# Performance work log

Hardware: AMD Instinct MI355X
Metric: run time of the kernel (lower is better)

## Reference

```python
import jax, jax.numpy as jnp
import numpy as np

B, N, C = 4, 2048, 512
H, D, L = 8, 64, 64  # num_heads, per-head dim, lunchbox_dim
SCALE = max(D, L) ** (-0.5)

def setup_inputs() -> dict:
    key = jax.random.key(0)
    k1, k2, k3, k4 = jax.random.split(key, 4)
    x = jax.random.normal(k1, (B, N, C), dtype=jnp.float32)
    v = jax.random.normal(k2, (N, H, L), dtype=jnp.float32) * (1.0 / np.sqrt(N))
    qkv = jax.random.normal(k3, (C, D * 2 * H), dtype=jnp.float32) * (1.0 / np.sqrt(C))
    proj = jax.random.normal(k4, (H * L, D), dtype=jnp.float32) * (1.0 / np.sqrt(H * L))
    return {"x": x, "v": v, "qkv": qkv, "proj": proj}

def reference(x, v, qkv, proj):
    # x: [B,N,C] -> [B,N,H,2,D]
    h = jnp.einsum('bnc,cd->bnd', x, qkv).reshape(B, N, H, 2, D)
    q = h[:, :, :, 0, :]  # [B,N,H,D]
    k = h[:, :, :, 1, :]  # [B,N,H,D]
    # attention scores [B,H,N,N]; NOTE: original code calls tf.nn.softmax but
    # discards the result, so no softmax is applied (faithful reproduction).
    attn = jnp.einsum('bnhd,bmhd->bhnm', q, k) * SCALE
    # contract with batch-independent lunchbox V: [B,H,N,N] x [N,H,L] -> [B,N,H,L]
    res = jnp.einsum('bhnm,mhl->bnhl', attn, v).reshape(B, N, H * L)
    out = jnp.einsum('bnc,cd->bnd', res, proj)  # [B,N,D]
    return out
```

## Files before the change

kernel.cpp:

```cpp
#include <hip/hip_runtime.h>
#include <hip/hip_bf16.h>


using f32x4 = __attribute__((ext_vector_type(4))) float;
using s16x8 = __attribute__((ext_vector_type(8))) short;

__device__ __forceinline__ unsigned short f2bf(float f) {
  unsigned int i;
  __builtin_memcpy(&i, &f, 4);
  unsigned int lsb = (i >> 16) & 1u;
  i += 0x7fffu + lsb;
  return (unsigned short)(i >> 16);
}
__device__ __forceinline__ float bf2f(unsigned short u) {
  unsigned int i = ((unsigned int)u) << 16;
  float f;
  __builtin_memcpy(&f, &i, 4);
  return f;
}
__device__ __forceinline__ void async_cp16(const void* g, void* l) {
  __builtin_amdgcn_global_load_lds((const __attribute__((address_space(1))) void*)g,
                                   (__attribute__((address_space(3))) void*)l, 16, 0, 0);
}

__global__ void k_prep(const float* __restrict__ x, const float* __restrict__ qkv,
                       unsigned short* __restrict__ xb, unsigned short* __restrict__ qkvT) {
  const int id = blockIdx.x;
  const int tid = threadIdx.x;
  if (id < 2048) {
    size_t i = ((size_t)id * 256 + tid) * 8;
    f32x4 a = *(const f32x4*)(x + i);
    f32x4 b = *(const f32x4*)(x + i + 4);
    ushort4 lo, hi;
    lo.x = f2bf(a[0]); lo.y = f2bf(a[1]); lo.z = f2bf(a[2]); lo.w = f2bf(a[3]);
    hi.x = f2bf(b[0]); hi.y = f2bf(b[1]); hi.z = f2bf(b[2]); hi.w = f2bf(b[3]);
    *(ushort4*)(xb + i) = lo;
    *(ushort4*)(xb + i + 4) = hi;
  } else {
    __shared__ float tile[32][33];
    const int idx = id - 2048;
    const int j0 = (idx & 31) * 32;
    const int c0 = (idx >> 5) * 32;
    const int tx = tid & 31, ty = tid >> 5;
#pragma unroll
    for (int i = 0; i < 32; i += 8)
      tile[ty + i][tx] = qkv[(size_t)(c0 + ty + i) * 1024 + j0 + tx];
    __syncthreads();
    const int h = j0 >> 7, s = (j0 >> 6) & 1, d0 = j0 & 63;
    const int jp0 = s * 512 + h * 64 + d0;
#pragma unroll
    for (int i = 0; i < 32; i += 8)
      qkvT[(size_t)(jp0 + ty + i) * 512 + c0 + tx] = f2bf(tile[tx][ty + i]);
  }
}

__global__ __launch_bounds__(512) void k_gemm1(
    const unsigned short* __restrict__ A,
    const unsigned short* __restrict__ Bt,
    unsigned short* __restrict__ Qws,
    unsigned short* __restrict__ Kws) {
  __shared__ unsigned short As[128 * 64];
  __shared__ unsigned short Bs[128 * 64];
  const int m0 = blockIdx.x * 128;
  const int n0 = blockIdx.y * 128;
  const int tid = threadIdx.x;
  const int lane = tid & 63;
  const int wave = tid >> 6;
  const int wm = wave >> 1, wn = wave & 1;

  f32x4 acc[2][4] = {};

  const int rlane = lane >> 3;
  const int clane = (lane & 7) * 8;

  for (int kt = 0; kt < 512; kt += 64) {
    __syncthreads();
#pragma unroll
    for (int i = 0; i < 2; ++i) {
      async_cp16(A + (size_t)(m0 + i * 64 + wave * 8 + rlane) * 512 + kt + clane,
                 As + (i * 64 + wave * 8) * 64);
      async_cp16(Bt + (size_t)(n0 + i * 64 + wave * 8 + rlane) * 512 + kt + clane,
                 Bs + (i * 64 + wave * 8) * 64);
    }
    __syncthreads();
#pragma unroll
    for (int kk = 0; kk < 64; kk += 32) {
      s16x8 af[2], bfr[4];
#pragma unroll
      for (int i = 0; i < 2; ++i)
        af[i] = *(const s16x8*)(As + (wm * 32 + i * 16 + (lane & 15)) * 64 + kk + (lane >> 4) * 8);
#pragma unroll
      for (int j = 0; j < 4; ++j)
        bfr[j] = *(const s16x8*)(Bs + (wn * 64 + j * 16 + (lane & 15)) * 64 + kk + (lane >> 4) * 8);
#pragma unroll
      for (int i = 0; i < 2; ++i)
#pragma unroll
        for (int j = 0; j < 4; ++j)
          acc[i][j] = __builtin_amdgcn_mfma_f32_16x16x32_bf16(af[i], bfr[j], acc[i][j], 0, 0, 0);
    }
  }
  const int n_base = n0 + wn * 64;
#pragma unroll
  for (int i = 0; i < 2; ++i) {
    int grow = m0 + wm * 32 + i * 16 + (lane >> 4) * 4;
#pragma unroll
    for (int j = 0; j < 4; ++j) {
      int gcol = n_base + j * 16 + (lane & 15);
      unsigned short* dst;
      float scale;
      if (gcol < 512) { dst = Qws; scale = 0.125f; }
      else            { dst = Kws; gcol -= 512; scale = 1.0f; }
#pragma unroll
      for (int r = 0; r < 4; ++r)
        dst[(size_t)(grow + r) * 512 + gcol] = f2bf(acc[i][j][r] * scale);
    }
  }
}

__global__ void k_kv_partial(const unsigned short* __restrict__ Kws,
                             const float* __restrict__ v,
                             float* __restrict__ KVp) {
  const int wg = blockIdx.x;
  const int chunk = wg & 15;
  const int h = (wg >> 4) & 7;
  const int b = wg >> 7;
  __shared__ unsigned short Ks[128 * 64];
  __shared__ float Vs[128 * 64];
  const int tid = threadIdx.x;
  const int lane = tid & 63;
  const int wave = tid >> 6;
  const int n0 = chunk * 128;
  {
    const int r = wave * 32 + (lane >> 3);
    const int c = (lane & 7) * 8;
#pragma unroll
    for (int i = 0; i < 4; ++i)
      async_cp16(Kws + (size_t)(b * 2048 + n0 + r + i * 8) * 512 + h * 64 + c,
                 Ks + (wave * 32 + i * 8) * 64);
  }
  {
    const int r = wave * 32 + (lane >> 4);
    const int c = (lane & 15) * 4;
#pragma unroll
    for (int i = 0; i < 8; ++i)
      async_cp16(v + (size_t)(n0 + r + i * 4) * 512 + h * 64 + c,
                 Vs + (wave * 32 + i * 4) * 64);
  }
  __syncthreads();
  const int dq0 = (tid & 15) * 4;
  const int l0 = (tid >> 4) * 4;
  float acc[4][4] = {};
#pragma unroll 4
  for (int n = 0; n < 128; ++n) {
    ushort4 ku = *(const ushort4*)(Ks + n * 64 + dq0);
    f32x4 va = *(const f32x4*)(Vs + n * 64 + l0);
    float ka[4] = {bf2f(ku.x), bf2f(ku.y), bf2f(ku.z), bf2f(ku.w)};
#pragma unroll
    for (int a = 0; a < 4; ++a)
#pragma unroll
      for (int c = 0; c < 4; ++c)
        acc[a][c] += ka[a] * va[c];
  }
  float* dst = KVp + (size_t)wg * 4096;
#pragma unroll
  for (int a = 0; a < 4; ++a) {
    f32x4 o;
    o[0] = acc[a][0]; o[1] = acc[a][1]; o[2] = acc[a][2]; o[3] = acc[a][3];
    *(f32x4*)(dst + (dq0 + a) * 64 + l0) = o;
  }
}

__global__ void k_kv_reduce_w(const float* __restrict__ KVp,
                              const float* __restrict__ proj,
                              unsigned short* __restrict__ WcatT) {
  const int bh = blockIdx.x;
  const int h = bh & 7;
  const int b = bh >> 3;
  __shared__ float kv[64 * 65];
  __shared__ float pj[64 * 64];
  const int tid = threadIdx.x;
#pragma unroll
  for (int j = 0; j < 16; ++j) {
    int e = tid + j * 256;
    float s = 0.f;
#pragma unroll
    for (int c = 0; c < 16; ++c)
      s += KVp[((size_t)bh * 16 + c) * 4096 + e];
    kv[(e >> 6) * 65 + (e & 63)] = s;
  }
#pragma unroll
  for (int j = 0; j < 16; ++j) {
    int e = tid + j * 256;
    pj[e] = proj[(size_t)(h * 64 + (e >> 6)) * 64 + (e & 63)];
  }
  __syncthreads();
  const int dq = tid >> 2;
  const int d0 = (tid & 3) * 16;
  f32x4 w[4] = {};
  for (int l = 0; l < 64; ++l) {
    float kvv = kv[dq * 65 + l];
#pragma unroll
    for (int jj = 0; jj < 4; ++jj) {
      f32x4 p4 = *(const f32x4*)(pj + l * 64 + d0 + jj * 4);
      w[jj] += kvv * p4;
    }
  }
#pragma unroll
  for (int jj = 0; jj < 4; ++jj)
#pragma unroll
    for (int q = 0; q < 4; ++q)
      WcatT[(size_t)(b * 64 + d0 + jj * 4 + q) * 512 + h * 64 + dq] = f2bf(w[jj][q]);
}

__global__ __launch_bounds__(64) void k_gemm2(
    const unsigned short* __restrict__ Qws,
    const unsigned short* __restrict__ WcatT,
    float* __restrict__ out) {
  const int m0 = blockIdx.x * 16;
  const int lane = threadIdx.x;
  const unsigned short* Bb = WcatT + (size_t)(m0 >> 11) * 64 * 512;
  const int arow = lane & 15;
  const int koff = (lane >> 4) * 8;
  f32x4 acc[4] = {};
#pragma unroll
  for (int kk = 0; kk < 16; ++kk) {
    s16x8 af = *(const s16x8*)(Qws + (size_t)(m0 + arow) * 512 + kk * 32 + koff);
#pragma unroll
    for (int j = 0; j < 4; ++j) {
      s16x8 bf = *(const s16x8*)(Bb + (size_t)(j * 16 + arow) * 512 + kk * 32 + koff);
      acc[j] = __builtin_amdgcn_mfma_f32_16x16x32_bf16(af, bf, acc[j], 0, 0, 0);
    }
  }
  const int grow = m0 + (lane >> 4) * 4;
#pragma unroll
  for (int j = 0; j < 4; ++j) {
    int gcol = j * 16 + arow;
#pragma unroll
    for (int r = 0; r < 4; ++r)
      out[(size_t)(grow + r) * 64 + gcol] = acc[j][r];
  }
}

extern "C" void kernel_launch(void* const* d_in, const int* in_sizes, int n_in,
                              void* d_out, int out_size, void* d_ws, size_t ws_size,
                              hipStream_t stream) {
  const float* x    = (const float*)d_in[0];
  const float* v    = (const float*)d_in[1];
  const float* qkv  = (const float*)d_in[2];
  const float* proj = (const float*)d_in[3];
  float* out = (float*)d_out;

  char* ws = (char*)d_ws;
  unsigned short* xb   = (unsigned short*)ws; ws += (size_t)8192 * 512 * 2;
  unsigned short* qkvT = (unsigned short*)ws; ws += (size_t)1024 * 512 * 2;
  unsigned short* Qws  = (unsigned short*)ws; ws += (size_t)8192 * 512 * 2;
  unsigned short* Kws  = (unsigned short*)ws; ws += (size_t)8192 * 512 * 2;
  float*          KVp  = (float*)ws;          ws += (size_t)512 * 4096 * 4;
  unsigned short* Wc   = (unsigned short*)ws; ws += (size_t)4 * 64 * 512 * 2;

  hipLaunchKernelGGL(k_prep, dim3(2560), dim3(256), 0, stream, x, qkv, xb, qkvT);
  hipLaunchKernelGGL(k_gemm1, dim3(64, 8), dim3(512), 0, stream, xb, qkvT, Qws, Kws);
  hipLaunchKernelGGL(k_kv_partial, dim3(512), dim3(256), 0, stream, Kws, v, KVp);
  hipLaunchKernelGGL(k_kv_reduce_w, dim3(32), dim3(256), 0, stream, KVp, proj, Wc);
  hipLaunchKernelGGL(k_gemm2, dim3(512), dim3(64), 0, stream, Qws, Wc, out);
}
```

Baseline: 118.7 us.

## Double-buffer gemm1 LDS tiles and reduce KV partials with atomics

The QKV GEMM now uses two LDS buffers, so the async global-to-LDS copy of the next K tile can overlap the MFMA work on the current tile. This removes one barrier per iteration. Separately, the per-chunk KV partial products are accumulated with float atomicAdd into a zeroed [32,64,64] buffer, which k_prep clears. This drops the 16-way partial reduction in the follow-up kernel and the large partial workspace. The atomics add contention (16 writers per address) and make the summation order nondeterministic.

```diff
diff --git a/kernel.cpp b/kernel.cpp
--- a/kernel.cpp
+++ b/kernel.cpp
@@ -24,7 +24,8 @@
 }
 
 __global__ void k_prep(const float* __restrict__ x, const float* __restrict__ qkv,
-                       unsigned short* __restrict__ xb, unsigned short* __restrict__ qkvT) {
+                       unsigned short* __restrict__ xb, unsigned short* __restrict__ qkvT,
+                       float* __restrict__ KV) {
   const int id = blockIdx.x;
   const int tid = threadIdx.x;
   if (id < 2048) {
@@ -36,7 +37,7 @@
     hi.x = f2bf(b[0]); hi.y = f2bf(b[1]); hi.z = f2bf(b[2]); hi.w = f2bf(b[3]);
     *(ushort4*)(xb + i) = lo;
     *(ushort4*)(xb + i + 4) = hi;
-  } else {
+  } else if (id < 2560) {
     __shared__ float tile[32][33];
     const int idx = id - 2048;
     const int j0 = (idx & 31) * 32;
@@ -51,6 +52,12 @@
 #pragma unroll
     for (int i = 0; i < 32; i += 8)
       qkvT[(size_t)(jp0 + ty + i) * 512 + c0 + tx] = f2bf(tile[tx][ty + i]);
+  } else {
+    float* dst = KV + (size_t)(id - 2560) * 4096;
+    f32x4 z = {0.f, 0.f, 0.f, 0.f};
+#pragma unroll
+    for (int j = 0; j < 4; ++j)
+      *(f32x4*)(dst + j * 1024 + tid * 4) = z;
   }
 }
 
@@ -59,8 +66,8 @@
     const unsigned short* __restrict__ Bt,
     unsigned short* __restrict__ Qws,
     unsigned short* __restrict__ Kws) {
-  __shared__ unsigned short As[128 * 64];
-  __shared__ unsigned short Bs[128 * 64];
+  __shared__ unsigned short As[2][128 * 64];
+  __shared__ unsigned short Bs[2][128 * 64];
   const int m0 = blockIdx.x * 128;
   const int n0 = blockIdx.y * 128;
   const int tid = threadIdx.x;
@@ -73,32 +80,46 @@
   const int rlane = lane >> 3;
   const int clane = (lane & 7) * 8;
 
-  for (int kt = 0; kt < 512; kt += 64) {
+#define STAGE(buf, kt)                                                              \
+  {                                                                                 \
+    _Pragma("unroll") for (int i = 0; i < 2; ++i) {                                 \
+      async_cp16(A + (size_t)(m0 + i * 64 + wave * 8 + rlane) * 512 + (kt) + clane, \
+                 As[buf] + (i * 64 + wave * 8) * 64);                               \
+      async_cp16(Bt + (size_t)(n0 + i * 64 + wave * 8 + rlane) * 512 + (kt) + clane,\
+                 Bs[buf] + (i * 64 + wave * 8) * 64);                               \
+    }                                                                               \
+  }
+
+#define COMPUTE(buf)                                                                       \
+  {                                                                                        \
+    _Pragma("unroll") for (int kk = 0; kk < 64; kk += 32) {                                \
+      s16x8 af[2], bfr[4];                                                                 \
+      _Pragma("unroll") for (int i = 0; i < 2; ++i)                                        \
+        af[i] = *(const s16x8*)(As[buf] + (wm * 32 + i * 16 + (lane & 15)) * 64 + kk +     \
+                                (lane >> 4) * 8);                                          \
+      _Pragma("unroll") for (int j = 0; j < 4; ++j)                                        \
+        bfr[j] = *(const s16x8*)(Bs[buf] + (wn * 64 + j * 16 + (lane & 15)) * 64 + kk +    \
+                                 (lane >> 4) * 8);                                         \
+      _Pragma("unroll") for (int i = 0; i < 2; ++i)                                        \
+        _Pragma("unroll") for (int j = 0; j < 4; ++j)                                      \
+          acc[i][j] = __builtin_amdgcn_mfma_f32_16x16x32_bf16(af[i], bfr[j], acc[i][j],    \
+                                                              0, 0, 0);                    \
+    }                                                                                      \
+  }
+
+  STAGE(0, 0);
+  __syncthreads();
+  int cur = 0;
+  for (int kt = 64; kt < 512; kt += 64) {
+    STAGE(cur ^ 1, kt);
+    COMPUTE(cur);
     __syncthreads();
-#pragma unroll
-    for (int i = 0; i < 2; ++i) {
-      async_cp16(A + (size_t)(m0 + i * 64 + wave * 8 + rlane) * 512 + kt + clane,
-                 As + (i * 64 + wave * 8) * 64);
-      async_cp16(Bt + (size_t)(n0 + i * 64 + wave * 8 + rlane) * 512 + kt + clane,
-                 Bs + (i * 64 + wave * 8) * 64);
-    }
-    __syncthreads();
-#pragma unroll
-    for (int kk = 0; kk < 64; kk += 32) {
-      s16x8 af[2], bfr[4];
-#pragma unroll
-      for (int i = 0; i < 2; ++i)
-        af[i] = *(const s16x8*)(As + (wm * 32 + i * 16 + (lane & 15)) * 64 + kk + (lane >> 4) * 8);
-#pragma unroll
-      for (int j = 0; j < 4; ++j)
-        bfr[j] = *(const s16x8*)(Bs + (wn * 64 + j * 16 + (lane & 15)) * 64 + kk + (lane >> 4) * 8);
-#pragma unroll
-      for (int i = 0; i < 2; ++i)
-#pragma unroll
-        for (int j = 0; j < 4; ++j)
-          acc[i][j] = __builtin_amdgcn_mfma_f32_16x16x32_bf16(af[i], bfr[j], acc[i][j], 0, 0, 0);
-    }
-  }
+    cur ^= 1;
+  }
+  COMPUTE(cur);
+#undef STAGE
+#undef COMPUTE
+
   const int n_base = n0 + wn * 64;
 #pragma unroll
   for (int i = 0; i < 2; ++i) {
@@ -119,7 +140,7 @@
 
 __global__ void k_kv_partial(const unsigned short* __restrict__ Kws,
                              const float* __restrict__ v,
-                             float* __restrict__ KVp) {
+                             float* __restrict__ KV) {
   const int wg = blockIdx.x;
   const int chunk = wg & 15;
   const int h = (wg >> 4) & 7;
@@ -161,18 +182,17 @@
       for (int c = 0; c < 4; ++c)
         acc[a][c] += ka[a] * va[c];
   }
-  float* dst = KVp + (size_t)wg * 4096;
-#pragma unroll
-  for (int a = 0; a < 4; ++a) {
-    f32x4 o;
-    o[0] = acc[a][0]; o[1] = acc[a][1]; o[2] = acc[a][2]; o[3] = acc[a][3];
-    *(f32x4*)(dst + (dq0 + a) * 64 + l0) = o;
-  }
-}
-
-__global__ void k_kv_reduce_w(const float* __restrict__ KVp,
-                              const float* __restrict__ proj,
-                              unsigned short* __restrict__ WcatT) {
+  float* dst = KV + (size_t)(b * 8 + h) * 4096;
+#pragma unroll
+  for (int a = 0; a < 4; ++a)
+#pragma unroll
+    for (int c = 0; c < 4; ++c)
+      atomicAdd(dst + (dq0 + a) * 64 + l0 + c, acc[a][c]);
+}
+
+__global__ void k_w(const float* __restrict__ KV,
+                    const float* __restrict__ proj,
+                    unsigned short* __restrict__ WcatT) {
   const int bh = blockIdx.x;
   const int h = bh & 7;
   const int b = bh >> 3;
@@ -182,11 +202,7 @@
 #pragma unroll
   for (int j = 0; j < 16; ++j) {
     int e = tid + j * 256;
-    float s = 0.f;
-#pragma unroll
-    for (int c = 0; c < 16; ++c)
-      s += KVp[((size_t)bh * 16 + c) * 4096 + e];
-    kv[(e >> 6) * 65 + (e & 63)] = s;
+    kv[(e >> 6) * 65 + (e & 63)] = KV[(size_t)bh * 4096 + e];
   }
 #pragma unroll
   for (int j = 0; j < 16; ++j) {
@@ -255,12 +271,12 @@
   unsigned short* qkvT = (unsigned short*)ws; ws += (size_t)1024 * 512 * 2;
   unsigned short* Qws  = (unsigned short*)ws; ws += (size_t)8192 * 512 * 2;
   unsigned short* Kws  = (unsigned short*)ws; ws += (size_t)8192 * 512 * 2;
-  float*          KVp  = (float*)ws;          ws += (size_t)512 * 4096 * 4;
+  float*          KV   = (float*)ws;          ws += (size_t)32 * 4096 * 4;
   unsigned short* Wc   = (unsigned short*)ws; ws += (size_t)4 * 64 * 512 * 2;
 
-  hipLaunchKernelGGL(k_prep, dim3(2560), dim3(256), 0, stream, x, qkv, xb, qkvT);
+  hipLaunchKernelGGL(k_prep, dim3(2592), dim3(256), 0, stream, x, qkv, xb, qkvT, KV);
   hipLaunchKernelGGL(k_gemm1, dim3(64, 8), dim3(512), 0, stream, xb, qkvT, Qws, Kws);
-  hipLaunchKernelGGL(k_kv_partial, dim3(512), dim3(256), 0, stream, Kws, v, KVp);
-  hipLaunchKernelGGL(k_kv_reduce_w, dim3(32), dim3(256), 0, stream, KVp, proj, Wc);
+  hipLaunchKernelGGL(k_kv_partial, dim3(512), dim3(256), 0, stream, Kws, v, KV);
+  hipLaunchKernelGGL(k_w, dim3(32), dim3(256), 0, stream, KV, proj, Wc);
   hipLaunchKernelGGL(k_gemm2, dim3(512), dim3(64), 0, stream, Qws, Wc, out);
 }
```

Result: slower. 137.6 us (+16.0%).

## Split KV-reduce/W kernel across more blocks and remap GEMM1 block order

Applied to the files above, without the earlier changes.

Rewrites the KV reduction plus projection kernel to use 256 blocks instead of 32: each block sums one 8-row slice of the KV partials and computes the matching slice of W. The aim is to raise occupancy on a kernel that previously ran on very few CUs. GEMM1 moves to a 1D grid with a remapped block index so that consecutive blocks sweep the M dimension within one N column, which could change L2 reuse of the A and B tiles. Each of the 8 blocks per head now reloads the full projection slice, adding some redundant global traffic.

```diff
diff --git a/kernel.cpp b/kernel.cpp
--- a/kernel.cpp
+++ b/kernel.cpp
@@ -61,8 +61,10 @@
     unsigned short* __restrict__ Kws) {
   __shared__ unsigned short As[128 * 64];
   __shared__ unsigned short Bs[128 * 64];
-  const int m0 = blockIdx.x * 128;
-  const int n0 = blockIdx.y * 128;
+  const int lin = blockIdx.x;
+  const int wg = (lin & 7) * 64 + (lin >> 3);
+  const int m0 = (wg >> 3) * 128;
+  const int n0 = (wg & 7) * 128;
   const int tid = threadIdx.x;
   const int lane = tid & 63;
   const int wave = tid >> 6;
@@ -170,46 +172,45 @@
   }
 }
 
-__global__ void k_kv_reduce_w(const float* __restrict__ KVp,
-                              const float* __restrict__ proj,
-                              unsigned short* __restrict__ WcatT) {
-  const int bh = blockIdx.x;
+__global__ void k_w(const float* __restrict__ KVp,
+                    const float* __restrict__ proj,
+                    unsigned short* __restrict__ WcatT) {
+  const int blk = blockIdx.x;
+  const int g = blk & 7;
+  const int bh = blk >> 3;
   const int h = bh & 7;
   const int b = bh >> 3;
-  __shared__ float kv[64 * 65];
+  __shared__ float kv[8 * 64];
   __shared__ float pj[64 * 64];
   const int tid = threadIdx.x;
+  {
+    const int e = tid * 2;
+    const float* src = KVp + (size_t)bh * 16 * 4096 + g * 512 + e;
+    float s0 = 0.f, s1 = 0.f;
+#pragma unroll
+    for (int c = 0; c < 16; ++c) {
+      float2 t = *(const float2*)(src + c * 4096);
+      s0 += t.x; s1 += t.y;
+    }
+    kv[e] = s0; kv[e + 1] = s1;
+  }
 #pragma unroll
   for (int j = 0; j < 16; ++j) {
     int e = tid + j * 256;
-    float s = 0.f;
-#pragma unroll
-    for (int c = 0; c < 16; ++c)
-      s += KVp[((size_t)bh * 16 + c) * 4096 + e];
-    kv[(e >> 6) * 65 + (e & 63)] = s;
-  }
-#pragma unroll
-  for (int j = 0; j < 16; ++j) {
-    int e = tid + j * 256;
-    pj[e] = proj[(size_t)(h * 64 + (e >> 6)) * 64 + (e & 63)];
+    pj[e] = proj[(size_t)h * 4096 + e];
   }
   __syncthreads();
-  const int dq = tid >> 2;
-  const int d0 = (tid & 3) * 16;
-  f32x4 w[4] = {};
+  const int dout = tid & 63;
+  const int dq0 = tid >> 6;
+  float w0 = 0.f, w1 = 0.f;
   for (int l = 0; l < 64; ++l) {
-    float kvv = kv[dq * 65 + l];
-#pragma unroll
-    for (int jj = 0; jj < 4; ++jj) {
-      f32x4 p4 = *(const f32x4*)(pj + l * 64 + d0 + jj * 4);
-      w[jj] += kvv * p4;
-    }
-  }
-#pragma unroll
-  for (int jj = 0; jj < 4; ++jj)
-#pragma unroll
-    for (int q = 0; q < 4; ++q)
-      WcatT[(size_t)(b * 64 + d0 + jj * 4 + q) * 512 + h * 64 + dq] = f2bf(w[jj][q]);
+    float p = pj[l * 64 + dout];
+    w0 += kv[dq0 * 64 + l] * p;
+    w1 += kv[(dq0 + 4) * 64 + l] * p;
+  }
+  const int dqb = h * 64 + g * 8;
+  WcatT[(size_t)(b * 64 + dout) * 512 + dqb + dq0] = f2bf(w0);
+  WcatT[(size_t)(b * 64 + dout) * 512 + dqb + dq0 + 4] = f2bf(w1);
 }
 
 __global__ __launch_bounds__(64) void k_gemm2(
@@ -259,8 +260,8 @@
   unsigned short* Wc   = (unsigned short*)ws; ws += (size_t)4 * 64 * 512 * 2;
 
   hipLaunchKernelGGL(k_prep, dim3(2560), dim3(256), 0, stream, x, qkv, xb, qkvT);
-  hipLaunchKernelGGL(k_gemm1, dim3(64, 8), dim3(512), 0, stream, xb, qkvT, Qws, Kws);
+  hipLaunchKernelGGL(k_gemm1, dim3(512), dim3(512), 0, stream, xb, qkvT, Qws, Kws);
   hipLaunchKernelGGL(k_kv_partial, dim3(512), dim3(256), 0, stream, Kws, v, KVp);
-  hipLaunchKernelGGL(k_kv_reduce_w, dim3(32), dim3(256), 0, stream, KVp, proj, Wc);
+  hipLaunchKernelGGL(k_w, dim3(256), dim3(256), 0, stream, KVp, proj, Wc);
   hipLaunchKernelGGL(k_gemm2, dim3(512), dim3(64), 0, stream, Qws, Wc, out);
 }
```

After: 112.5 us. 1.06x faster.

## Fuse K^T·V and projection into single MFMA kernel with transposed K/V layouts

Applied to the files above, without the earlier changes.

Replaces the scalar FP32 K^T·V partial-sum kernel and its separate reduce/projection kernel with one MFMA-based kernel per (batch, head). To feed it, gemm1 now writes K transposed and the prep kernel also writes bf16 transposed copies of v and proj. gemm1 also remaps block indices so neighbouring workgroups share tiles. The aim is to remove the FP32 partial buffer round trip and one kernel launch. In exchange the fused kernel runs only 32 workgroups, each streaming 2048-long rows directly from global memory without LDS staging, and v and the K·V product are now rounded to bf16.

```diff
diff --git a/kernel.cpp b/kernel.cpp
--- a/kernel.cpp
+++ b/kernel.cpp
@@ -12,11 +12,10 @@
   i += 0x7fffu + lsb;
   return (unsigned short)(i >> 16);
 }
-__device__ __forceinline__ float bf2f(unsigned short u) {
-  unsigned int i = ((unsigned int)u) << 16;
-  float f;
-  __builtin_memcpy(&f, &i, 4);
-  return f;
+__device__ __forceinline__ ushort4 pk4(f32x4 a) {
+  ushort4 u;
+  u.x = f2bf(a[0]); u.y = f2bf(a[1]); u.z = f2bf(a[2]); u.w = f2bf(a[3]);
+  return u;
 }
 __device__ __forceinline__ void async_cp16(const void* g, void* l) {
   __builtin_amdgcn_global_load_lds((const __attribute__((address_space(1))) void*)g,
@@ -24,7 +23,9 @@
 }
 
 __global__ void k_prep(const float* __restrict__ x, const float* __restrict__ qkv,
-                       unsigned short* __restrict__ xb, unsigned short* __restrict__ qkvT) {
+                       const float* __restrict__ v, const float* __restrict__ proj,
+                       unsigned short* __restrict__ xb, unsigned short* __restrict__ qkvT,
+                       unsigned short* __restrict__ VT, unsigned short* __restrict__ projT) {
   const int id = blockIdx.x;
   const int tid = threadIdx.x;
   if (id < 2048) {
@@ -36,12 +37,14 @@
     hi.x = f2bf(b[0]); hi.y = f2bf(b[1]); hi.z = f2bf(b[2]); hi.w = f2bf(b[3]);
     *(ushort4*)(xb + i) = lo;
     *(ushort4*)(xb + i + 4) = hi;
-  } else {
-    __shared__ float tile[32][33];
+    return;
+  }
+  __shared__ float tile[32][33];
+  const int tx = tid & 31, ty = tid >> 5;
+  if (id < 2560) {
     const int idx = id - 2048;
     const int j0 = (idx & 31) * 32;
     const int c0 = (idx >> 5) * 32;
-    const int tx = tid & 31, ty = tid >> 5;
 #pragma unroll
     for (int i = 0; i < 32; i += 8)
       tile[ty + i][tx] = qkv[(size_t)(c0 + ty + i) * 1024 + j0 + tx];
@@ -51,6 +54,28 @@
 #pragma unroll
     for (int i = 0; i < 32; i += 8)
       qkvT[(size_t)(jp0 + ty + i) * 512 + c0 + tx] = f2bf(tile[tx][ty + i]);
+  } else if (id < 3584) {
+    const int idx = id - 2560;
+    const int j0 = (idx & 15) * 32;
+    const int n0 = (idx >> 4) * 32;
+#pragma unroll
+    for (int i = 0; i < 32; i += 8)
+      tile[ty + i][tx] = v[(size_t)(n0 + ty + i) * 512 + j0 + tx];
+    __syncthreads();
+#pragma unroll
+    for (int i = 0; i < 32; i += 8)
+      VT[(size_t)(j0 + ty + i) * 2048 + n0 + tx] = f2bf(tile[tx][ty + i]);
+  } else {
+    const int idx = id - 3584;
+    const int d0 = (idx & 1) * 32;
+    const int j0 = (idx >> 1) * 32;
+#pragma unroll
+    for (int i = 0; i < 32; i += 8)
+      tile[ty + i][tx] = proj[(size_t)(j0 + ty + i) * 64 + d0 + tx];
+    __syncthreads();
+#pragma unroll
+    for (int i = 0; i < 32; i += 8)
+      projT[(size_t)(d0 + ty + i) * 512 + j0 + tx] = f2bf(tile[tx][ty + i]);
   }
 }
 
@@ -58,11 +83,13 @@
     const unsigned short* __restrict__ A,
     const unsigned short* __restrict__ Bt,
     unsigned short* __restrict__ Qws,
-    unsigned short* __restrict__ Kws) {
+    unsigned short* __restrict__ KwsT) {
   __shared__ unsigned short As[128 * 64];
   __shared__ unsigned short Bs[128 * 64];
-  const int m0 = blockIdx.x * 128;
-  const int n0 = blockIdx.y * 128;
+  const int lin = blockIdx.x;
+  const int wg = (lin & 7) * 64 + (lin >> 3);
+  const int m0 = (wg >> 3) * 128;
+  const int n0 = (wg & 7) * 128;
   const int tid = threadIdx.x;
   const int lane = tid & 63;
   const int wave = tid >> 6;
@@ -100,116 +127,84 @@
     }
   }
   const int n_base = n0 + wn * 64;
-#pragma unroll
-  for (int i = 0; i < 2; ++i) {
-    int grow = m0 + wm * 32 + i * 16 + (lane >> 4) * 4;
-#pragma unroll
-    for (int j = 0; j < 4; ++j) {
-      int gcol = n_base + j * 16 + (lane & 15);
-      unsigned short* dst;
-      float scale;
-      if (gcol < 512) { dst = Qws; scale = 0.125f; }
-      else            { dst = Kws; gcol -= 512; scale = 1.0f; }
-#pragma unroll
-      for (int r = 0; r < 4; ++r)
-        dst[(size_t)(grow + r) * 512 + gcol] = f2bf(acc[i][j][r] * scale);
-    }
-  }
-}
-
-__global__ void k_kv_partial(const unsigned short* __restrict__ Kws,
-                             const float* __restrict__ v,
-                             float* __restrict__ KVp) {
-  const int wg = blockIdx.x;
-  const int chunk = wg & 15;
-  const int h = (wg >> 4) & 7;
-  const int b = wg >> 7;
-  __shared__ unsigned short Ks[128 * 64];
-  __shared__ float Vs[128 * 64];
+  if (n_base < 512) {
+#pragma unroll
+    for (int i = 0; i < 2; ++i) {
+      int grow = m0 + wm * 32 + i * 16 + (lane >> 4) * 4;
+#pragma unroll
+      for (int j = 0; j < 4; ++j) {
+        int gcol = n_base + j * 16 + (lane & 15);
+#pragma unroll
+        for (int r = 0; r < 4; ++r)
+          Qws[(size_t)(grow + r) * 512 + gcol] = f2bf(acc[i][j][r] * 0.125f);
+      }
+    }
+  } else {
+#pragma unroll
+    for (int i = 0; i < 2; ++i) {
+      int grow = m0 + wm * 32 + i * 16 + (lane >> 4) * 4;
+      int b = grow >> 11, n = grow & 2047;
+#pragma unroll
+      for (int j = 0; j < 4; ++j) {
+        int dfull = n_base - 512 + j * 16 + (lane & 15);
+        *(ushort4*)(KwsT + (size_t)(b * 512 + dfull) * 2048 + n) = pk4(acc[i][j]);
+      }
+    }
+  }
+}
+
+__global__ __launch_bounds__(256) void k_kv_w(
+    const unsigned short* __restrict__ KwsT,
+    const unsigned short* __restrict__ VT,
+    const unsigned short* __restrict__ projT,
+    unsigned short* __restrict__ WcatT) {
+  const int bh = blockIdx.x;
+  const int h = bh & 7;
+  const int b = bh >> 3;
   const int tid = threadIdx.x;
   const int lane = tid & 63;
   const int wave = tid >> 6;
-  const int n0 = chunk * 128;
-  {
-    const int r = wave * 32 + (lane >> 3);
-    const int c = (lane & 7) * 8;
-#pragma unroll
-    for (int i = 0; i < 4; ++i)
-      async_cp16(Kws + (size_t)(b * 2048 + n0 + r + i * 8) * 512 + h * 64 + c,
-                 Ks + (wave * 32 + i * 8) * 64);
-  }
-  {
-    const int r = wave * 32 + (lane >> 4);
-    const int c = (lane & 15) * 4;
-#pragma unroll
-    for (int i = 0; i < 8; ++i)
-      async_cp16(v + (size_t)(n0 + r + i * 4) * 512 + h * 64 + c,
-                 Vs + (wave * 32 + i * 4) * 64);
+  const int arow = wave * 16 + (lane & 15);
+  const int koff = (lane >> 4) * 8;
+  const unsigned short* Ab = KwsT + (size_t)bh * 64 * 2048;
+  const unsigned short* Bb = VT + (size_t)h * 64 * 2048;
+
+  f32x4 acc[4] = {};
+#pragma unroll 4
+  for (int kk = 0; kk < 64; ++kk) {
+    s16x8 af = *(const s16x8*)(Ab + (size_t)arow * 2048 + kk * 32 + koff);
+#pragma unroll
+    for (int j = 0; j < 4; ++j) {
+      s16x8 bf = *(const s16x8*)(Bb + (size_t)(j * 16 + (lane & 15)) * 2048 + kk * 32 + koff);
+      acc[j] = __builtin_amdgcn_mfma_f32_16x16x32_bf16(af, bf, acc[j], 0, 0, 0);
+    }
+  }
+  __shared__ unsigned short kvl[64][80];
+#pragma unroll
+  for (int j = 0; j < 4; ++j) {
+    int row = wave * 16 + (lane >> 4) * 4;
+    int col = j * 16 + (lane & 15);
+#pragma unroll
+    for (int r = 0; r < 4; ++r)
+      kvl[row + r][col] = f2bf(acc[j][r]);
   }
   __syncthreads();
-  const int dq0 = (tid & 15) * 4;
-  const int l0 = (tid >> 4) * 4;
-  float acc[4][4] = {};
-#pragma unroll 4
-  for (int n = 0; n < 128; ++n) {
-    ushort4 ku = *(const ushort4*)(Ks + n * 64 + dq0);
-    f32x4 va = *(const f32x4*)(Vs + n * 64 + l0);
-    float ka[4] = {bf2f(ku.x), bf2f(ku.y), bf2f(ku.z), bf2f(ku.w)};
-#pragma unroll
-    for (int a = 0; a < 4; ++a)
-#pragma unroll
-      for (int c = 0; c < 4; ++c)
-        acc[a][c] += ka[a] * va[c];
-  }
-  float* dst = KVp + (size_t)wg * 4096;
-#pragma unroll
-  for (int a = 0; a < 4; ++a) {
-    f32x4 o;
-    o[0] = acc[a][0]; o[1] = acc[a][1]; o[2] = acc[a][2]; o[3] = acc[a][3];
-    *(f32x4*)(dst + (dq0 + a) * 64 + l0) = o;
-  }
-}
-
-__global__ void k_kv_reduce_w(const float* __restrict__ KVp,
-                              const float* __restrict__ proj,
-                              unsigned short* __restrict__ WcatT) {
-  const int bh = blockIdx.x;
-  const int h = bh & 7;
-  const int b = bh >> 3;
-  __shared__ float kv[64 * 65];
-  __shared__ float pj[64 * 64];
-  const int tid = threadIdx.x;
-#pragma unroll
-  for (int j = 0; j < 16; ++j) {
-    int e = tid + j * 256;
-    float s = 0.f;
-#pragma unroll
-    for (int c = 0; c < 16; ++c)
-      s += KVp[((size_t)bh * 16 + c) * 4096 + e];
-    kv[(e >> 6) * 65 + (e & 63)] = s;
-  }
-#pragma unroll
-  for (int j = 0; j < 16; ++j) {
-    int e = tid + j * 256;
-    pj[e] = proj[(size_t)(h * 64 + (e >> 6)) * 64 + (e & 63)];
-  }
-  __syncthreads();
-  const int dq = tid >> 2;
-  const int d0 = (tid & 3) * 16;
-  f32x4 w[4] = {};
-  for (int l = 0; l < 64; ++l) {
-    float kvv = kv[dq * 65 + l];
-#pragma unroll
-    for (int jj = 0; jj < 4; ++jj) {
-      f32x4 p4 = *(const f32x4*)(pj + l * 64 + d0 + jj * 4);
-      w[jj] += kvv * p4;
-    }
-  }
-#pragma unroll
-  for (int jj = 0; jj < 4; ++jj)
-#pragma unroll
-    for (int q = 0; q < 4; ++q)
-      WcatT[(size_t)(b * 64 + d0 + jj * 4 + q) * 512 + h * 64 + dq] = f2bf(w[jj][q]);
+  f32x4 wacc[4] = {};
+#pragma unroll
+  for (int kk = 0; kk < 2; ++kk) {
+    s16x8 af = *(const s16x8*)(&kvl[arow][kk * 32 + koff]);
+#pragma unroll
+    for (int j = 0; j < 4; ++j) {
+      s16x8 bf = *(const s16x8*)(projT + (size_t)(j * 16 + (lane & 15)) * 512 + h * 64 + kk * 32 + koff);
+      wacc[j] = __builtin_amdgcn_mfma_f32_16x16x32_bf16(af, bf, wacc[j], 0, 0, 0);
+    }
+  }
+  const int dq = wave * 16 + (lane >> 4) * 4;
+#pragma unroll
+  for (int j = 0; j < 4; ++j) {
+    int dout = j * 16 + (lane & 15);
+    *(ushort4*)(WcatT + (size_t)(b * 64 + dout) * 512 + h * 64 + dq) = pk4(wacc[j]);
+  }
 }
 
 __global__ __launch_bounds__(64) void k_gemm2(
@@ -251,16 +246,16 @@
   float* out = (float*)d_out;
 
   char* ws = (char*)d_ws;
-  unsigned short* xb   = (unsigned short*)ws; ws += (size_t)8192 * 512 * 2;
-  unsigned short* qkvT = (unsigned short*)ws; ws += (size_t)1024 * 512 * 2;
-  unsigned short* Qws  = (unsigned short*)ws; ws += (size_t)8192 * 512 * 2;
-  unsigned short* Kws  = (unsigned short*)ws; ws += (size_t)8192 * 512 * 2;
-  float*          KVp  = (float*)ws;          ws += (size_t)512 * 4096 * 4;
-  unsigned short* Wc   = (unsigned short*)ws; ws += (size_t)4 * 64 * 512 * 2;
-
-  hipLaunchKernelGGL(k_prep, dim3(2560), dim3(256), 0, stream, x, qkv, xb, qkvT);
-  hipLaunchKernelGGL(k_gemm1, dim3(64, 8), dim3(512), 0, stream, xb, qkvT, Qws, Kws);
-  hipLaunchKernelGGL(k_kv_partial, dim3(512), dim3(256), 0, stream, Kws, v, KVp);
-  hipLaunchKernelGGL(k_kv_reduce_w, dim3(32), dim3(256), 0, stream, KVp, proj, Wc);
+  unsigned short* xb    = (unsigned short*)ws; ws += (size_t)8192 * 512 * 2;
+  unsigned short* qkvT  = (unsigned short*)ws; ws += (size_t)1024 * 512 * 2;
+  unsigned short* Qws   = (unsigned short*)ws; ws += (size_t)8192 * 512 * 2;
+  unsigned short* KwsT  = (unsigned short*)ws; ws += (size_t)8192 * 512 * 2;
+  unsigned short* VT    = (unsigned short*)ws; ws += (size_t)512 * 2048 * 2;
+  unsigned short* projT = (unsigned short*)ws; ws += (size_t)64 * 512 * 2;
+  unsigned short* Wc    = (unsigned short*)ws; ws += (size_t)4 * 64 * 512 * 2;
+
+  hipLaunchKernelGGL(k_prep, dim3(3616), dim3(256), 0, stream, x, qkv, v, proj, xb, qkvT, VT, projT);
+  hipLaunchKernelGGL(k_gemm1, dim3(512), dim3(512), 0, stream, xb, qkvT, Qws, KwsT);
+  hipLaunchKernelGGL(k_kv_w, dim3(32), dim3(256), 0, stream, KwsT, VT, projT, Wc);
   hipLaunchKernelGGL(k_gemm2, dim3(512), dim3(64), 0, stream, Qws, Wc, out);
 }
```

Measured after the change: 139.1 us. 1.17x slower.
